# Kernel tuning notes

Hardware: AMD Instinct MI355X
Metric: run time of the kernel (lower is better)

The kernel has to match this reference:

```python
import jax, jax.numpy as jnp
import numpy as np

N = 100000          # nodes
E = 1600000         # edges
F_IN = 128          # in_channels
C = 32              # hidden_channels (per head)
H = 4               # heads
NEG_SLOPE = 0.2     # PyG GATConv default leaky_relu slope


def setup_inputs() -> dict:
    key = jax.random.key(0)
    ks = jax.random.split(key, 6)
    x = jax.random.normal(ks[0], (N, F_IN), dtype=jnp.float32)
    edge_index = jax.random.randint(ks[1], (2, E), 0, N, dtype=jnp.int32)
    # learned params (PyG GATConv: lin weight, att_src, att_dst, bias)
    W = jax.random.normal(ks[2], (F_IN, H * C), dtype=jnp.float32) * (1.0 / np.sqrt(F_IN))
    att_src = jax.random.normal(ks[3], (H, C), dtype=jnp.float32) * 0.1
    att_dst = jax.random.normal(ks[4], (H, C), dtype=jnp.float32) * 0.1
    bias = jnp.zeros((H * C,), dtype=jnp.float32)
    return {"x": x, "edge_index": edge_index, "W": W,
            "att_src": att_src, "att_dst": att_dst, "bias": bias}


def reference(x, edge_index, W, att_src, att_dst, bias):
    # linear projection, split into heads: [N, H, C]
    h = (x @ W).reshape(N, H, C)
    # per-node attention terms: [N, H]
    a_src = jnp.einsum('nhc,hc->nh', h, att_src)
    a_dst = jnp.einsum('nhc,hc->nh', h, att_dst)
    src, dst = edge_index[0], edge_index[1]
    # edge-wise logits: [E, H]
    alpha = jax.nn.leaky_relu(a_src[src] + a_dst[dst], NEG_SLOPE)
    # segment softmax over incoming edges of each dst node
    amax = jax.ops.segment_max(alpha, dst, num_segments=N)       # [N, H]
    amax = jnp.where(jnp.isfinite(amax), amax, 0.0)
    ex = jnp.exp(alpha - amax[dst])                              # [E, H]
    denom = jax.ops.segment_sum(ex, dst, num_segments=N)         # [N, H]
    alpha = ex / (denom[dst] + 1e-16)                            # [E, H]
    # weighted messages, scatter-add to dst: [N, H, C]
    msg = h[src] * alpha[:, :, None]
    out = jax.ops.segment_sum(msg, dst, num_segments=N)
    out = out.reshape(N, H * C) + bias
    return jax.nn.elu(out)
```

## Files before the change

### kernel.cpp

```cpp
#include <hip/hip_runtime.h>
#include <hip/hip_bf16.h>
#include <math.h>

#define N_NODES 100000
#define N_EDGES 1600000
#define NEG_SLOPE 0.2f

#define NB_BUCKET 782
#define ST_CAP 2560

#define OFF_H     0
#define OFF_ASRC  25600000
#define OFF_ADST  27200000
#define OFF_OFFS  28800000
#define OFF_BCNT  29200128
#define OFF_BOFF  29204224
#define OFF_BCUR  29208320
#define OFF_TMP   29212416
#define OFF_CSR   35612416

__device__ __forceinline__ float leaky(float x) {
    return fmaxf(x, NEG_SLOPE * x);
}
__device__ __forceinline__ unsigned int pack_bf2(float a, float b) {
    unsigned int ua = (unsigned int)__bfloat16_as_ushort(__float2bfloat16(a));
    unsigned int ub = (unsigned int)__bfloat16_as_ushort(__float2bfloat16(b));
    return ua | (ub << 16);
}
__device__ __forceinline__ float bf_lo(unsigned int u) {
    return __uint_as_float(u << 16);
}
__device__ __forceinline__ float bf_hi(unsigned int u) {
    return __uint_as_float(u & 0xffff0000u);
}

#define BR2 128
__global__ __launch_bounds__(256, 2) void gemm_att_kernel(
    const float* __restrict__ x, const float* __restrict__ W,
    const float* __restrict__ att_src, const float* __restrict__ att_dst,
    uint4* __restrict__ h4, float* __restrict__ a_src, float* __restrict__ a_dst)
{
    __shared__ float xs[32][BR2 + 4];
    __shared__ float ws[32][132];

    const int tid = threadIdx.x;
    const int cx  = tid & 15;
    const int ry  = tid >> 4;
    const int n0  = blockIdx.x * BR2;

    float acc[8][8];
#pragma unroll
    for (int i = 0; i < 8; ++i)
#pragma unroll
        for (int j = 0; j < 8; ++j) acc[i][j] = 0.f;

    const int xr  = tid >> 1;
    const int xk0 = (tid & 1) * 16;
    const int wk  = tid >> 3;
    const int wc0 = (tid & 7) * 16;

    for (int k0 = 0; k0 < 128; k0 += 32) {
        {
            int row = n0 + xr;
            row = row < N_NODES ? row : N_NODES - 1;
            const float4* xp = (const float4*)&x[(size_t)row * 128 + k0 + xk0];
#pragma unroll
            for (int i = 0; i < 4; ++i) {
                const float4 v = xp[i];
                xs[xk0 + i * 4 + 0][xr] = v.x;
                xs[xk0 + i * 4 + 1][xr] = v.y;
                xs[xk0 + i * 4 + 2][xr] = v.z;
                xs[xk0 + i * 4 + 3][xr] = v.w;
            }
        }
        {
            const float4* wp = (const float4*)&W[(size_t)(k0 + wk) * 128 + wc0];
#pragma unroll
            for (int i = 0; i < 4; ++i)
                *(float4*)&ws[wk][wc0 + i * 4] = wp[i];
        }
        __syncthreads();

#pragma unroll 2
        for (int k = 0; k < 32; ++k) {
            const float4 xa = *(const float4*)&xs[k][ry * 8];
            const float4 xb = *(const float4*)&xs[k][ry * 8 + 4];
            const float4 wa = *(const float4*)&ws[k][cx * 8];
            const float4 wb = *(const float4*)&ws[k][cx * 8 + 4];
            const float xv[8] = {xa.x, xa.y, xa.z, xa.w, xb.x, xb.y, xb.z, xb.w};
            const float wv[8] = {wa.x, wa.y, wa.z, wa.w, wb.x, wb.y, wb.z, wb.w};
#pragma unroll
            for (int i = 0; i < 8; ++i)
#pragma unroll
                for (int j = 0; j < 8; ++j)
                    acc[i][j] = fmaf(xv[i], wv[j], acc[i][j]);
        }
        __syncthreads();
    }

    float as8[8], ad8[8];
    {
        const float4 a0 = ((const float4*)att_src)[cx * 2];
        const float4 a1 = ((const float4*)att_src)[cx * 2 + 1];
        const float4 b0 = ((const float4*)att_dst)[cx * 2];
        const float4 b1 = ((const float4*)att_dst)[cx * 2 + 1];
        as8[0]=a0.x; as8[1]=a0.y; as8[2]=a0.z; as8[3]=a0.w;
        as8[4]=a1.x; as8[5]=a1.y; as8[6]=a1.z; as8[7]=a1.w;
        ad8[0]=b0.x; ad8[1]=b0.y; ad8[2]=b0.z; ad8[3]=b0.w;
        ad8[4]=b1.x; ad8[5]=b1.y; ad8[6]=b1.z; ad8[7]=b1.w;
    }
    const int head = cx >> 2;

#pragma unroll
    for (int i = 0; i < 8; ++i) {
        const int row = n0 + ry * 8 + i;
        if (row >= N_NODES) break;
        uint4 pk;
        pk.x = pack_bf2(acc[i][0], acc[i][1]);
        pk.y = pack_bf2(acc[i][2], acc[i][3]);
        pk.z = pack_bf2(acc[i][4], acc[i][5]);
        pk.w = pack_bf2(acc[i][6], acc[i][7]);
        h4[(size_t)row * 16 + cx] = pk;

        float vs = 0.f, vd = 0.f;
#pragma unroll
        for (int c = 0; c < 8; ++c) {
            vs = fmaf(acc[i][c], as8[c], vs);
            vd = fmaf(acc[i][c], ad8[c], vd);
        }
        vs += __shfl_xor(vs, 1); vd += __shfl_xor(vd, 1);
        vs += __shfl_xor(vs, 2); vd += __shfl_xor(vd, 2);
        if ((cx & 3) == 0) {
            a_src[row * 4 + head] = vs;
            a_dst[row * 4 + head] = vd;
        }
    }
}

#define BH_EPB 3125
__global__ __launch_bounds__(256) void bucket_hist_kernel(
    const int* __restrict__ dst, int* __restrict__ bcnt)
{
    __shared__ int cnt[NB_BUCKET];
    const int tid = threadIdx.x;
    for (int i = tid; i < NB_BUCKET; i += 256) cnt[i] = 0;
    __syncthreads();
    const int e0 = blockIdx.x * BH_EPB;
    for (int i = tid; i < BH_EPB; i += 256)
        atomicAdd(&cnt[dst[e0 + i] >> 7], 1);
    __syncthreads();
    for (int i = tid; i < NB_BUCKET; i += 256)
        if (cnt[i]) atomicAdd(&bcnt[i], cnt[i]);
}

__global__ __launch_bounds__(1024) void bucket_scan_kernel(
    const int* __restrict__ bcnt, int* __restrict__ boff, int* __restrict__ bcur)
{
    const int tid  = threadIdx.x;
    const int lane = tid & 63;
    const int wv   = tid >> 6;
    const int v    = (tid < NB_BUCKET) ? bcnt[tid] : 0;

    int sv = v;
#pragma unroll
    for (int off = 1; off < 64; off <<= 1) {
        int u = __shfl_up(sv, off);
        if (lane >= off) sv += u;
    }
    __shared__ int wsum[16];
    if (lane == 63) wsum[wv] = sv;
    __syncthreads();
    if (tid == 0) {
        int run = 0;
#pragma unroll
        for (int k = 0; k < 16; ++k) { int t = wsum[k]; wsum[k] = run; run += t; }
    }
    __syncthreads();
    if (tid < NB_BUCKET) {
        const int excl = wsum[wv] + sv - v;
        boff[tid] = excl;
        bcur[tid] = excl;
    }
    if (tid == 0) boff[NB_BUCKET] = N_EDGES;
}

#define S1_EPB 3125
__global__ __launch_bounds__(256) void scat1_kernel(
    const int* __restrict__ src, const int* __restrict__ dst,
    int* __restrict__ bcur, unsigned int* __restrict__ tmp)
{
    __shared__ int cnt[NB_BUCKET];
    const int tid = threadIdx.x;
    for (int i = tid; i < NB_BUCKET; i += 256) cnt[i] = 0;
    __syncthreads();
    const int e0 = blockIdx.x * S1_EPB;
    for (int i = tid; i < S1_EPB; i += 256)
        atomicAdd(&cnt[dst[e0 + i] >> 7], 1);
    __syncthreads();
    for (int b = tid; b < NB_BUCKET; b += 256) {
        const int c = cnt[b];
        cnt[b] = c ? atomicAdd(&bcur[b], c) : 0;
    }
    __syncthreads();
    for (int i = tid; i < S1_EPB; i += 256) {
        const int d = dst[e0 + i];
        const int s = src[e0 + i];
        const int p = atomicAdd(&cnt[d >> 7], 1);
        tmp[p] = ((unsigned int)s << 7) | (unsigned int)(d & 127);
    }
}

__global__ __launch_bounds__(256) void phaseB_kernel(
    const unsigned int* __restrict__ tmp, const int* __restrict__ boff,
    int* __restrict__ offs, int* __restrict__ csr)
{
    __shared__ unsigned int st[ST_CAP];
    __shared__ int hist[128];
    __shared__ int cur[128];
    __shared__ int wtot[4];

    const int b    = blockIdx.x;
    const int tid  = threadIdx.x;
    const int lane = tid & 63;
    const int wv   = tid >> 6;
    const int base = boff[b];
    const int cnt  = boff[b + 1] - base;

    if (tid < 128) hist[tid] = 0;
    __syncthreads();

    for (int i = tid; i < cnt; i += 256) {
        const unsigned int v = tmp[base + i];
        if (i < ST_CAP) st[i] = v;
        atomicAdd(&hist[v & 127], 1);
    }
    __syncthreads();

    const int hv = (tid < 128) ? hist[tid] : 0;
    int sv = hv;
#pragma unroll
    for (int off = 1; off < 64; off <<= 1) {
        int u = __shfl_up(sv, off);
        if (lane >= off) sv += u;
    }
    if (lane == 63) wtot[wv] = sv;
    __syncthreads();
    const int wpre = (wv > 0 ? wtot[0] : 0) + (wv > 1 ? wtot[1] : 0);
    if (tid < 128) {
        const int excl = wpre + sv - hv;
        cur[tid] = excl;
        const int node = (b << 7) + tid;
        if (node < N_NODES) offs[node] = base + excl;
    }
    if (b == 0 && tid == 0) offs[N_NODES] = N_EDGES;
    __syncthreads();

    for (int i = tid; i < cnt; i += 256) {
        const unsigned int v = (i < ST_CAP) ? st[i] : tmp[base + i];
        const int p = atomicAdd(&cur[v & 127], 1);
        csr[base + p] = (int)(v >> 7);
    }
}

__global__ __launch_bounds__(256) void gat_agg_kernel(
    const int* __restrict__ csr_src, const int* __restrict__ offs,
    const uint4* __restrict__ h4,
    const float* __restrict__ a_src, const float* __restrict__ a_dst,
    const float* __restrict__ bias, float* __restrict__ out)
{
    __shared__ float2 st[4][4][68];
    __shared__ int s_nch[4];

    const int wv   = threadIdx.x >> 6;
    const int lane = threadIdx.x & 63;
    const int node = blockIdx.x * 4 + wv;
    const int q    = lane >> 4;
    const int l16  = lane & 15;
    const int hq   = l16 >> 2;

    const int start = offs[node];
    const int deg   = offs[node + 1] - start;
    const float4 ad4 = ((const float4*)a_dst)[node];

    if (lane == 0) s_nch[wv] = (deg + 63) >> 6;
    __syncthreads();
    const int cmax = max(max(s_nch[0], s_nch[1]), max(s_nch[2], s_nch[3]));

    float acc[8];
#pragma unroll
    for (int c = 0; c < 8; ++c) acc[c] = 0.f;
    float den = 0.f;

    for (int ch = 0; ch < cmax; ++ch) {
        const int base = ch << 6;
        const int rem  = deg - base;

        float sf = 0.f, e0 = 0.f, e1 = 0.f, e2 = 0.f, e3 = 0.f;
        if (lane < rem) {
            const int s = csr_src[start + base + lane];
            sf = __int_as_float(s);
            const float4 as4 = ((const float4*)a_src)[s];
            e0 = __expf(leaky(as4.x + ad4.x));
            e1 = __expf(leaky(as4.y + ad4.y));
            e2 = __expf(leaky(as4.z + ad4.z));
            e3 = __expf(leaky(as4.w + ad4.w));
        }
        st[wv][0][lane] = make_float2(sf, e0);
        st[wv][1][lane] = make_float2(sf, e1);
        st[wv][2][lane] = make_float2(sf, e2);
        st[wv][3][lane] = make_float2(sf, e3);
        __syncthreads();

        const int cnt4 = rem > 0 ? ((rem > 64 ? 64 : (rem + 3) & ~3)) : 0;
        const float2* sp = &st[wv][hq][q];
        for (int j = 0; j < cnt4; j += 4) {
            const float2 se = sp[j];
            const unsigned int soff =
                (__float_as_uint(se.x) << 4) + (unsigned int)l16;
            const uint4 hv = h4[soff];
            const float ex = se.y;
            acc[0] = fmaf(bf_lo(hv.x), ex, acc[0]);
            acc[1] = fmaf(bf_hi(hv.x), ex, acc[1]);
            acc[2] = fmaf(bf_lo(hv.y), ex, acc[2]);
            acc[3] = fmaf(bf_hi(hv.y), ex, acc[3]);
            acc[4] = fmaf(bf_lo(hv.z), ex, acc[4]);
            acc[5] = fmaf(bf_hi(hv.z), ex, acc[5]);
            acc[6] = fmaf(bf_lo(hv.w), ex, acc[6]);
            acc[7] = fmaf(bf_hi(hv.w), ex, acc[7]);
            den += ex;
        }
        __syncthreads();
    }

#pragma unroll
    for (int c = 0; c < 8; ++c) {
        acc[c] += __shfl_xor(acc[c], 16);
        acc[c] += __shfl_xor(acc[c], 32);
    }
    den += __shfl_xor(den, 16);
    den += __shfl_xor(den, 32);

    if (q == 0) {
        const float inv = 1.0f / (den + 1e-16f);
        const float4 b0 = ((const float4*)bias)[l16 * 2];
        const float4 b1 = ((const float4*)bias)[l16 * 2 + 1];
        float o[8];
        o[0] = acc[0] * inv + b0.x; o[1] = acc[1] * inv + b0.y;
        o[2] = acc[2] * inv + b0.z; o[3] = acc[3] * inv + b0.w;
        o[4] = acc[4] * inv + b1.x; o[5] = acc[5] * inv + b1.y;
        o[6] = acc[6] * inv + b1.z; o[7] = acc[7] * inv + b1.w;
#pragma unroll
        for (int c = 0; c < 8; ++c)
            o[c] = o[c] > 0.f ? o[c] : expm1f(o[c]);
        float4* op = (float4*)&out[(size_t)node * 128 + l16 * 8];
        op[0] = make_float4(o[0], o[1], o[2], o[3]);
        op[1] = make_float4(o[4], o[5], o[6], o[7]);
    }
}

extern "C" void kernel_launch(void* const* d_in, const int* in_sizes, int n_in,
                              void* d_out, int out_size, void* d_ws, size_t ws_size,
                              hipStream_t stream)
{
    const float* x       = (const float*)d_in[0];
    const int*   ei      = (const int*)  d_in[1];
    const float* W       = (const float*)d_in[2];
    const float* att_src = (const float*)d_in[3];
    const float* att_dst = (const float*)d_in[4];
    const float* bias    = (const float*)d_in[5];
    float*       out     = (float*)d_out;

    char* ws = (char*)d_ws;
    uint4* h4    = (uint4*)(ws + OFF_H);
    float* a_src = (float*)(ws + OFF_ASRC);
    float* a_dst = (float*)(ws + OFF_ADST);
    int*   offs  = (int*)  (ws + OFF_OFFS);
    int*   bcnt  = (int*)  (ws + OFF_BCNT);
    int*   boff  = (int*)  (ws + OFF_BOFF);
    int*   bcur  = (int*)  (ws + OFF_BCUR);
    unsigned int* tmp = (unsigned int*)(ws + OFF_TMP);
    int*   csr   = (int*)  (ws + OFF_CSR);

    const int* srcp = ei;
    const int* dstp = ei + N_EDGES;

    hipMemsetAsync(bcnt, 0, NB_BUCKET * sizeof(int), stream);

    gemm_att_kernel<<<(N_NODES + BR2 - 1) / BR2, 256, 0, stream>>>(
        x, W, att_src, att_dst, h4, a_src, a_dst);

    bucket_hist_kernel<<<N_EDGES / BH_EPB, 256, 0, stream>>>(dstp, bcnt);
    bucket_scan_kernel<<<1, 1024, 0, stream>>>(bcnt, boff, bcur);
    scat1_kernel<<<N_EDGES / S1_EPB, 256, 0, stream>>>(srcp, dstp, bcur, tmp);
    phaseB_kernel<<<NB_BUCKET, 256, 0, stream>>>(tmp, boff, offs, csr);

    gat_agg_kernel<<<N_NODES / 4, 256, 0, stream>>>(
        csr, offs, h4, a_src, a_dst, bias, out);
}
```

Measured before the change: 300.1 us.

## Replace FP32 SIMT projection GEMM with split-bf16 MFMA GEMM

Replaces the shared-memory FP32 FMA GEMM with a matrix-core kernel using 16x16x32 bf16 MFMA. Both x and W are split into hi/lo bf16 parts and combined with three MFMAs to keep close-to-fp32 accuracy. A small pre-kernel packs W into fragment layout each call. The attention dot products are now reduced through lane shuffles, and h is stored as scalar bf16 writes instead of packed uint4 stores, which may be less coalesced.

```diff
diff --git a/kernel.cpp b/kernel.cpp
--- a/kernel.cpp
+++ b/kernel.cpp
@@ -16,123 +16,151 @@
 #define OFF_BCNT  29200128
 #define OFF_BOFF  29204224
 #define OFF_BCUR  29208320
-#define OFF_TMP   29212416
-#define OFF_CSR   35612416
+#define OFF_WHI   29212416
+#define OFF_WLO   29245184
+#define OFF_TMP   29277952
+#define OFF_CSR   35677952
+
+typedef short short8 __attribute__((ext_vector_type(8)));
+typedef float floatx4 __attribute__((ext_vector_type(4)));
 
 __device__ __forceinline__ float leaky(float x) {
     return fmaxf(x, NEG_SLOPE * x);
 }
-__device__ __forceinline__ unsigned int pack_bf2(float a, float b) {
-    unsigned int ua = (unsigned int)__bfloat16_as_ushort(__float2bfloat16(a));
-    unsigned int ub = (unsigned int)__bfloat16_as_ushort(__float2bfloat16(b));
-    return ua | (ub << 16);
-}
 __device__ __forceinline__ float bf_lo(unsigned int u) {
     return __uint_as_float(u << 16);
 }
 __device__ __forceinline__ float bf_hi(unsigned int u) {
     return __uint_as_float(u & 0xffff0000u);
 }
-
-#define BR2 128
-__global__ __launch_bounds__(256, 2) void gemm_att_kernel(
-    const float* __restrict__ x, const float* __restrict__ W,
-    const float* __restrict__ att_src, const float* __restrict__ att_dst,
-    uint4* __restrict__ h4, float* __restrict__ a_src, float* __restrict__ a_dst)
-{
-    __shared__ float xs[32][BR2 + 4];
-    __shared__ float ws[32][132];
-
-    const int tid = threadIdx.x;
-    const int cx  = tid & 15;
-    const int ry  = tid >> 4;
-    const int n0  = blockIdx.x * BR2;
-
-    float acc[8][8];
-#pragma unroll
-    for (int i = 0; i < 8; ++i)
-#pragma unroll
-        for (int j = 0; j < 8; ++j) acc[i][j] = 0.f;
-
-    const int xr  = tid >> 1;
-    const int xk0 = (tid & 1) * 16;
-    const int wk  = tid >> 3;
-    const int wc0 = (tid & 7) * 16;
-
-    for (int k0 = 0; k0 < 128; k0 += 32) {
-        {
-            int row = n0 + xr;
-            row = row < N_NODES ? row : N_NODES - 1;
-            const float4* xp = (const float4*)&x[(size_t)row * 128 + k0 + xk0];
-#pragma unroll
-            for (int i = 0; i < 4; ++i) {
-                const float4 v = xp[i];
-                xs[xk0 + i * 4 + 0][xr] = v.x;
-                xs[xk0 + i * 4 + 1][xr] = v.y;
-                xs[xk0 + i * 4 + 2][xr] = v.z;
-                xs[xk0 + i * 4 + 3][xr] = v.w;
+__device__ __forceinline__ void split_pack(float a0, float a1,
+                                           unsigned int& hi, unsigned int& lo) {
+    const unsigned int u0 = __float_as_uint(a0);
+    const unsigned int u1 = __float_as_uint(a1);
+    hi = (u0 >> 16) | (u1 & 0xffff0000u);
+    const float l0 = a0 - __uint_as_float(u0 & 0xffff0000u);
+    const float l1 = a1 - __uint_as_float(u1 & 0xffff0000u);
+    lo = (__float_as_uint(l0) >> 16) | (__float_as_uint(l1) & 0xffff0000u);
+}
+
+__global__ __launch_bounds__(256) void wfrag_kernel(
+    const float* __restrict__ W, uint4* __restrict__ whi, uint4* __restrict__ wlo)
+{
+    const int t    = blockIdx.x * 256 + threadIdx.x;
+    const int lane = t & 63;
+    const int nt   = (t >> 6) & 7;
+    const int kt   = t >> 9;
+    const int c    = lane & 15;
+    const int quad = lane >> 4;
+    const int n    = nt * 16 + c;
+    const int k0   = kt * 32 + quad * 8;
+
+    unsigned int hu[4], lu[4];
+#pragma unroll
+    for (int j = 0; j < 4; ++j) {
+        const float a0 = W[(size_t)(k0 + 2 * j) * 128 + n];
+        const float a1 = W[(size_t)(k0 + 2 * j + 1) * 128 + n];
+        split_pack(a0, a1, hu[j], lu[j]);
+    }
+    whi[(kt * 8 + nt) * 64 + lane] = make_uint4(hu[0], hu[1], hu[2], hu[3]);
+    wlo[(kt * 8 + nt) * 64 + lane] = make_uint4(lu[0], lu[1], lu[2], lu[3]);
+}
+
+__global__ __launch_bounds__(512, 1) void gemm_mfma_kernel(
+    const float* __restrict__ x, const uint4* __restrict__ whi,
+    const uint4* __restrict__ wlo, const float* __restrict__ att_src,
+    const float* __restrict__ att_dst, unsigned short* __restrict__ h_bf,
+    float* __restrict__ a_src, float* __restrict__ a_dst)
+{
+    const int wave = threadIdx.x >> 6;
+    const int lane = threadIdx.x & 63;
+    const int rw   = wave >> 1;
+    const int cw   = wave & 1;
+    const int row0 = blockIdx.x * 256 + rw * 64;
+    const int c    = lane & 15;
+    const int quad = lane >> 4;
+
+    floatx4 acc[4][4];
+#pragma unroll
+    for (int i = 0; i < 4; ++i)
+#pragma unroll
+        for (int j = 0; j < 4; ++j) acc[i][j] = (floatx4){0.f, 0.f, 0.f, 0.f};
+
+    for (int kt = 0; kt < 4; ++kt) {
+        short8 ahi[4], alo[4];
+#pragma unroll
+        for (int rt = 0; rt < 4; ++rt) {
+            int r = row0 + rt * 16 + c;
+            if (r >= N_NODES) r = N_NODES - 1;
+            const float4* xp = (const float4*)&x[(size_t)r * 128 + kt * 32 + quad * 8];
+            const float4 v0 = xp[0];
+            const float4 v1 = xp[1];
+            const float xv[8] = {v0.x, v0.y, v0.z, v0.w, v1.x, v1.y, v1.z, v1.w};
+            union { short8 v; unsigned int u[4]; } H, L;
+#pragma unroll
+            for (int j = 0; j < 4; ++j)
+                split_pack(xv[2 * j], xv[2 * j + 1], H.u[j], L.u[j]);
+            ahi[rt] = H.v;
+            alo[rt] = L.v;
+        }
+#pragma unroll
+        for (int nt = 0; nt < 4; ++nt) {
+            const int nti = cw * 4 + nt;
+            union { uint4 q; short8 v; } BH, BL;
+            BH.q = whi[(kt * 8 + nti) * 64 + lane];
+            BL.q = wlo[(kt * 8 + nti) * 64 + lane];
+#pragma unroll
+            for (int rt = 0; rt < 4; ++rt) {
+                acc[rt][nt] = __builtin_amdgcn_mfma_f32_16x16x32_bf16(
+                    ahi[rt], BH.v, acc[rt][nt], 0, 0, 0);
+                acc[rt][nt] = __builtin_amdgcn_mfma_f32_16x16x32_bf16(
+                    alo[rt], BH.v, acc[rt][nt], 0, 0, 0);
+                acc[rt][nt] = __builtin_amdgcn_mfma_f32_16x16x32_bf16(
+                    ahi[rt], BL.v, acc[rt][nt], 0, 0, 0);
             }
         }
-        {
-            const float4* wp = (const float4*)&W[(size_t)(k0 + wk) * 128 + wc0];
-#pragma unroll
-            for (int i = 0; i < 4; ++i)
-                *(float4*)&ws[wk][wc0 + i * 4] = wp[i];
-        }
-        __syncthreads();
-
-#pragma unroll 2
-        for (int k = 0; k < 32; ++k) {
-            const float4 xa = *(const float4*)&xs[k][ry * 8];
-            const float4 xb = *(const float4*)&xs[k][ry * 8 + 4];
-            const float4 wa = *(const float4*)&ws[k][cx * 8];
-            const float4 wb = *(const float4*)&ws[k][cx * 8 + 4];
-            const float xv[8] = {xa.x, xa.y, xa.z, xa.w, xb.x, xb.y, xb.z, xb.w};
-            const float wv[8] = {wa.x, wa.y, wa.z, wa.w, wb.x, wb.y, wb.z, wb.w};
-#pragma unroll
-            for (int i = 0; i < 8; ++i)
-#pragma unroll
-                for (int j = 0; j < 8; ++j)
-                    acc[i][j] = fmaf(xv[i], wv[j], acc[i][j]);
-        }
-        __syncthreads();
-    }
-
-    float as8[8], ad8[8];
-    {
-        const float4 a0 = ((const float4*)att_src)[cx * 2];
-        const float4 a1 = ((const float4*)att_src)[cx * 2 + 1];
-        const float4 b0 = ((const float4*)att_dst)[cx * 2];
-        const float4 b1 = ((const float4*)att_dst)[cx * 2 + 1];
-        as8[0]=a0.x; as8[1]=a0.y; as8[2]=a0.z; as8[3]=a0.w;
-        as8[4]=a1.x; as8[5]=a1.y; as8[6]=a1.z; as8[7]=a1.w;
-        ad8[0]=b0.x; ad8[1]=b0.y; ad8[2]=b0.z; ad8[3]=b0.w;
-        ad8[4]=b1.x; ad8[5]=b1.y; ad8[6]=b1.z; ad8[7]=b1.w;
-    }
-    const int head = cx >> 2;
-
-#pragma unroll
-    for (int i = 0; i < 8; ++i) {
-        const int row = n0 + ry * 8 + i;
-        if (row >= N_NODES) break;
-        uint4 pk;
-        pk.x = pack_bf2(acc[i][0], acc[i][1]);
-        pk.y = pack_bf2(acc[i][2], acc[i][3]);
-        pk.z = pack_bf2(acc[i][4], acc[i][5]);
-        pk.w = pack_bf2(acc[i][6], acc[i][7]);
-        h4[(size_t)row * 16 + cx] = pk;
-
-        float vs = 0.f, vd = 0.f;
-#pragma unroll
-        for (int c = 0; c < 8; ++c) {
-            vs = fmaf(acc[i][c], as8[c], vs);
-            vd = fmaf(acc[i][c], ad8[c], vd);
-        }
-        vs += __shfl_xor(vs, 1); vd += __shfl_xor(vd, 1);
-        vs += __shfl_xor(vs, 2); vd += __shfl_xor(vd, 2);
-        if ((cx & 3) == 0) {
-            a_src[row * 4 + head] = vs;
-            a_dst[row * 4 + head] = vd;
+    }
+
+    const int cb = cw * 64;
+    float asv[4], adv[4];
+#pragma unroll
+    for (int nt = 0; nt < 4; ++nt) {
+        asv[nt] = att_src[cb + nt * 16 + c];
+        adv[nt] = att_dst[cb + nt * 16 + c];
+    }
+
+#pragma unroll
+    for (int rt = 0; rt < 4; ++rt) {
+        const int rbase = row0 + rt * 16 + quad * 4;
+#pragma unroll
+        for (int reg = 0; reg < 4; ++reg) {
+            const int row = rbase + reg;
+            if (row < N_NODES) {
+#pragma unroll
+                for (int nt = 0; nt < 4; ++nt)
+                    h_bf[(size_t)row * 128 + cb + nt * 16 + c] =
+                        __bfloat16_as_ushort(__float2bfloat16(acc[rt][nt][reg]));
+            }
+        }
+#pragma unroll
+        for (int hl = 0; hl < 2; ++hl) {
+#pragma unroll
+            for (int reg = 0; reg < 4; ++reg) {
+                float ps = acc[rt][2 * hl][reg] * asv[2 * hl]
+                         + acc[rt][2 * hl + 1][reg] * asv[2 * hl + 1];
+                float pd = acc[rt][2 * hl][reg] * adv[2 * hl]
+                         + acc[rt][2 * hl + 1][reg] * adv[2 * hl + 1];
+#pragma unroll
+                for (int off = 1; off < 16; off <<= 1) {
+                    ps += __shfl_xor(ps, off);
+                    pd += __shfl_xor(pd, off);
+                }
+                const int row = rbase + reg;
+                if (c == 0 && row < N_NODES) {
+                    a_src[row * 4 + 2 * cw + hl] = ps;
+                    a_dst[row * 4 + 2 * cw + hl] = pd;
+                }
+            }
         }
     }
 }
@@ -371,6 +399,7 @@
     float*       out     = (float*)d_out;
 
     char* ws = (char*)d_ws;
+    unsigned short* h_bf = (unsigned short*)(ws + OFF_H);
     uint4* h4    = (uint4*)(ws + OFF_H);
     float* a_src = (float*)(ws + OFF_ASRC);
     float* a_dst = (float*)(ws + OFF_ADST);
@@ -378,6 +407,8 @@
     int*   bcnt  = (int*)  (ws + OFF_BCNT);
     int*   boff  = (int*)  (ws + OFF_BOFF);
     int*   bcur  = (int*)  (ws + OFF_BCUR);
+    uint4* whi   = (uint4*)(ws + OFF_WHI);
+    uint4* wlo   = (uint4*)(ws + OFF_WLO);
     unsigned int* tmp = (unsigned int*)(ws + OFF_TMP);
     int*   csr   = (int*)  (ws + OFF_CSR);
 
@@ -386,8 +417,9 @@
 
     hipMemsetAsync(bcnt, 0, NB_BUCKET * sizeof(int), stream);
 
-    gemm_att_kernel<<<(N_NODES + BR2 - 1) / BR2, 256, 0, stream>>>(
-        x, W, att_src, att_dst, h4, a_src, a_dst);
+    wfrag_kernel<<<8, 256, 0, stream>>>(W, whi, wlo);
+    gemm_mfma_kernel<<<(N_NODES + 255) / 256, 512, 0, stream>>>(
+        x, whi, wlo, att_src, att_dst, h_bf, a_src, a_dst);
 
     bucket_hist_kernel<<<N_EDGES / BH_EPB, 256, 0, stream>>>(dstp, bcnt);
     bucket_scan_kernel<<<1, 1024, 0, stream>>>(bcnt, boff, bcur);
```

Measured after the change: 298.4 us. About the same (-0.6%).
